# Kernel optimization log

Hardware: AMD Instinct MI355X
Metric: run time of the kernel (lower is better)

Reference implementation:

```python
import jax, jax.numpy as jnp
from jax import lax
import numpy as np

_DN = ('NCHW', 'OIHW', 'NCHW')


def _upfirdn2d(x, f, up, down, padding, gain, flip_filter):
    """Reference upfirdn2d with a separable 1-D FIR filter f. padding=(px0,px1,py0,py1)."""
    N, C, H, W = x.shape
    if up > 1:
        # zero-stuff upsample
        x = x.reshape(N, C, H, 1, W, 1)
        x = jnp.pad(x, ((0, 0), (0, 0), (0, 0), (0, up - 1), (0, 0), (0, up - 1)))
        x = x.reshape(N, C, H * up, W * up)
    px0, px1, py0, py1 = padding
    x = jnp.pad(x, ((0, 0), (0, 0), (max(py0, 0), max(py1, 0)), (max(px0, 0), max(px1, 0))))
    x = x[:, :, max(-py0, 0): x.shape[2] - max(-py1, 0), max(-px0, 0): x.shape[3] - max(-px1, 0)]
    # 1-D filter gets gain**(ndim/2) per pass -> total gain after H and W passes
    f = f * (gain ** (f.ndim / 2))
    if not flip_filter:
        f = f[::-1]
    f = f.astype(x.dtype)
    kt = f.shape[0]
    # separable depthwise FIR: vertical then horizontal
    fy = jnp.broadcast_to(f.reshape(1, 1, kt, 1), (C, 1, kt, 1))
    x = lax.conv_general_dilated(x, fy, (1, 1), 'VALID', feature_group_count=C, dimension_numbers=_DN)
    fx = jnp.broadcast_to(f.reshape(1, 1, 1, kt), (C, 1, 1, kt))
    x = lax.conv_general_dilated(x, fx, (1, 1), 'VALID', feature_group_count=C, dimension_numbers=_DN)
    if down > 1:
        x = x[:, :, ::down, ::down]
    return x


def conv2d_resample(x, w, f, up, down, padding, groups, flip_weight, flip_filter):
    out_c, in_cpg, kh, kw = w.shape
    fh = fw = f.shape[0]
    px0 = px1 = py0 = py1 = int(padding)
    # adjust padding for up/downsampling (StyleGAN2-ADA conv2d_resample)
    if up > 1:
        px0 += (fw + up - 1) // 2
        px1 += (fw - up) // 2
        py0 += (fh + up - 1) // 2
        py1 += (fh - up) // 2
    if down > 1:
        px0 += (fw - down + 1) // 2
        px1 += (fw - down) // 2
        py0 += (fh - down + 1) // 2
        py1 += (fh - down) // 2
    # generic path: upsample+FIR+pad, grouped conv, then FIR+downsample
    ff = f if up > 1 else jnp.ones((1,), x.dtype)
    x = _upfirdn2d(x, ff, up, 1, (px0, px1, py0, py1), up * up, flip_filter)
    if not flip_weight:
        w = w[:, :, ::-1, ::-1]
    y = lax.conv_general_dilated(x, w, (1, 1), 'VALID', feature_group_count=groups, dimension_numbers=_DN)
    if down > 1:
        y = _upfirdn2d(y, f, 1, down, (0, 0, 0, 0), 1, flip_filter)
    return y


def setup_inputs() -> dict:
    key = jax.random.key(0)
    k1, k2, k3 = jax.random.split(key, 3)
    x = jax.random.normal(k1, (4, 128, 256, 256), dtype=jnp.float32)
    f = jax.random.uniform(k2, (4,), dtype=jnp.float32)
    f = f / jnp.sum(f)  # normalized FIR taps (like binomial [1,3,3,1]/8)
    w = jax.random.normal(k3, (128, 16, 3, 3), dtype=jnp.float32) * 0.05
    return {"x": x, "f": f, "w": w, "up": 2, "down": 1, "padding": 1,
            "groups": 8, "flip_weight": 1, "flip_filter": 0}


def reference(x, f, w, up, down, padding, groups, flip_weight, flip_filter):
    return conv2d_resample(x, w, f, up, down, padding, groups, flip_weight, flip_filter)
```

## Files before the change

### kernel.cpp

```cpp
#include <hip/hip_runtime.h>

#define N_BATCH 4
#define OC 128
#define ICPG 16
#define GROUPS 8
#define H 256
#define W 256

__device__ float g_weff[OC * ICPG * 9 * 4];


__global__ void prep_weff(const float* __restrict__ w, const float* __restrict__ f) {
    int t = blockIdx.x * 256 + threadIdx.x;
    if (t >= OC * ICPG) return;
    float wl[9];
#pragma unroll
    for (int i = 0; i < 9; i++) wl[i] = w[t * 9 + i];
    float fl[4];
#pragma unroll
    for (int i = 0; i < 4; i++) fl[i] = f[i];
    float* out = g_weff + t * 36;
#pragma unroll
    for (int r = 0; r < 3; r++) {
#pragma unroll
        for (int s = 0; s < 3; s++) {
#pragma unroll
            for (int pi = 0; pi < 2; pi++) {
#pragma unroll
                for (int pj = 0; pj < 2; pj++) {
                    float acc = 0.f;
#pragma unroll
                    for (int dy = 0; dy < 3; dy++) {
                        int fy = pi + dy - 2 * (r - 1);
                        if (fy < 0 || fy > 3) continue;
#pragma unroll
                        for (int dx = 0; dx < 3; dx++) {
                            int fx = pj + dx - 2 * (s - 1);
                            if (fx < 0 || fx > 3) continue;
                            acc += wl[dy * 3 + dx] * fl[fy] * fl[fx];
                        }
                    }
                    out[(r * 3 + s) * 4 + pi * 2 + pj] = 4.f * acc;
                }
            }
        }
    }
}

__global__ __launch_bounds__(256) void conv_fused(const float* __restrict__ x,
                                                  float* __restrict__ y) {
    const int bj = threadIdx.x;
    const int bi = blockIdx.x;
    const int o  = blockIdx.y;
    const int n  = blockIdx.z;
    const int g  = o >> 4;

    const float* xb = x + ((size_t)(n * OC + g * ICPG)) * (H * W);
    const float* wp = g_weff + (size_t)o * ICPG * 36;

    float acc0 = 0.f, acc1 = 0.f, acc2 = 0.f, acc3 = 0.f;

    for (int c = 0; c < ICPG; c++) {
        const float* xc = xb + (size_t)c * (H * W);
#pragma unroll
        for (int r = 0; r < 3; r++) {
            const int iy = bi + r - 1;
            const bool vy = (unsigned)iy < (unsigned)H;
            const float* xr = xc + iy * W;
#pragma unroll
            for (int s = 0; s < 3; s++) {
                const int ix = bj + s - 1;
                const float xv = (vy && (unsigned)ix < (unsigned)W) ? xr[ix] : 0.f;
                const float4 wv = *(const float4*)(wp + ((c * 3 + r) * 3 + s) * 4);
                acc0 += xv * wv.x;
                acc1 += xv * wv.y;
                acc2 += xv * wv.z;
                acc3 += xv * wv.w;
            }
        }
    }

    float* yb = y + (((size_t)(n * OC + o) * 512) + 2 * bi) * 512 + 2 * bj;
    *(float2*)(yb)       = make_float2(acc0, acc1);
    *(float2*)(yb + 512) = make_float2(acc2, acc3);
}

extern "C" void kernel_launch(void* const* d_in, const int* in_sizes, int n_in,
                              void* d_out, int out_size, void* d_ws, size_t ws_size,
                              hipStream_t stream) {
    const float* x = (const float*)d_in[0];
    const float* f = (const float*)d_in[1];
    const float* w = (const float*)d_in[2];
    float* y = (float*)d_out;

    hipLaunchKernelGGL(prep_weff, dim3(8), dim3(256), 0, stream, w, f);

    dim3 grid(H, OC, N_BATCH);
    hipLaunchKernelGGL(conv_fused, grid, dim3(256), 0, stream, x, y);
}
```

Before: 1.222 ms.

## Register-block 4 columns per thread with float4 loads and wave shuffles for halos

Each thread now computes four adjacent input columns, so one float4 load per input row replaces nine scalar loads. The left and right halo values come from neighbouring lanes via shuffles. Each weight float4 is reused across four columns and results are written with float4 stores. Blocks become 4 waves, each looping over 4 rows, which cuts the grid by 16x. The aim is less global load traffic and fewer instructions, in exchange for more registers per thread and fewer blocks.

```diff
diff --git a/kernel.cpp b/kernel.cpp
--- a/kernel.cpp
+++ b/kernel.cpp
@@ -6,6 +6,8 @@
 #define GROUPS 8
 #define H 256
 #define W 256
+#define TR 16
+#define RPW 4
 
 __device__ float g_weff[OC * ICPG * 9 * 4];
 
@@ -49,40 +51,68 @@
 
 __global__ __launch_bounds__(256) void conv_fused(const float* __restrict__ x,
                                                   float* __restrict__ y) {
-    const int bj = threadIdx.x;
-    const int bi = blockIdx.x;
-    const int o  = blockIdx.y;
-    const int n  = blockIdx.z;
-    const int g  = o >> 4;
+    const int lane = threadIdx.x & 63;
+    const int wid  = threadIdx.x >> 6;
+    const int rowt = blockIdx.x;
+    const int o    = blockIdx.y;
+    const int n    = blockIdx.z;
+    const int g    = o >> 4;
 
+    const int bj4 = lane << 2;
     const float* xb = x + ((size_t)(n * OC + g * ICPG)) * (H * W);
     const float* wp = g_weff + (size_t)o * ICPG * 36;
 
-    float acc0 = 0.f, acc1 = 0.f, acc2 = 0.f, acc3 = 0.f;
+    const int bi0 = rowt * TR + wid * RPW;
 
-    for (int c = 0; c < ICPG; c++) {
-        const float* xc = xb + (size_t)c * (H * W);
+#pragma unroll 1
+    for (int rr = 0; rr < RPW; rr++) {
+        const int bi = bi0 + rr;
+
+        float acc[4][4];
 #pragma unroll
-        for (int r = 0; r < 3; r++) {
-            const int iy = bi + r - 1;
-            const bool vy = (unsigned)iy < (unsigned)H;
-            const float* xr = xc + iy * W;
+        for (int j = 0; j < 4; j++)
 #pragma unroll
-            for (int s = 0; s < 3; s++) {
-                const int ix = bj + s - 1;
-                const float xv = (vy && (unsigned)ix < (unsigned)W) ? xr[ix] : 0.f;
-                const float4 wv = *(const float4*)(wp + ((c * 3 + r) * 3 + s) * 4);
-                acc0 += xv * wv.x;
-                acc1 += xv * wv.y;
-                acc2 += xv * wv.z;
-                acc3 += xv * wv.w;
+            for (int ph = 0; ph < 4; ph++) acc[j][ph] = 0.f;
+
+#pragma unroll 2
+        for (int c = 0; c < ICPG; c++) {
+            const float* xc = xb + (size_t)c * (H * W);
+            const float* wc = wp + c * 36;
+#pragma unroll
+            for (int r = 0; r < 3; r++) {
+                const int iy = bi + r - 1;
+                float4 v;
+                if ((unsigned)iy < (unsigned)H) {
+                    v = *(const float4*)(xc + (size_t)iy * W + bj4);
+                } else {
+                    v = make_float4(0.f, 0.f, 0.f, 0.f);
+                }
+                float xl = __shfl_up(v.w, 1);
+                if (lane == 0) xl = 0.f;
+                float xr = __shfl_down(v.x, 1);
+                if (lane == 63) xr = 0.f;
+                const float xw[6] = {xl, v.x, v.y, v.z, v.w, xr};
+#pragma unroll
+                for (int s = 0; s < 3; s++) {
+                    const float4 wv = *(const float4*)(wc + (r * 3 + s) * 4);
+#pragma unroll
+                    for (int j = 0; j < 4; j++) {
+                        const float xv = xw[j + s];
+                        acc[j][0] += xv * wv.x;
+                        acc[j][1] += xv * wv.y;
+                        acc[j][2] += xv * wv.z;
+                        acc[j][3] += xv * wv.w;
+                    }
+                }
             }
         }
+
+        float* yb = y + (((size_t)(n * OC + o) * (2 * H)) + 2 * bi) * (2 * W) + 2 * bj4;
+        *(float4*)(yb)             = make_float4(acc[0][0], acc[0][1], acc[1][0], acc[1][1]);
+        *(float4*)(yb + 4)         = make_float4(acc[2][0], acc[2][1], acc[3][0], acc[3][1]);
+        *(float4*)(yb + 2 * W)     = make_float4(acc[0][2], acc[0][3], acc[1][2], acc[1][3]);
+        *(float4*)(yb + 2 * W + 4) = make_float4(acc[2][2], acc[2][3], acc[3][2], acc[3][3]);
     }
-
-    float* yb = y + (((size_t)(n * OC + o) * 512) + 2 * bi) * 512 + 2 * bj;
-    *(float2*)(yb)       = make_float2(acc0, acc1);
-    *(float2*)(yb + 512) = make_float2(acc2, acc3);
 }
 
 extern "C" void kernel_launch(void* const* d_in, const int* in_sizes, int n_in,
@@ -95,6 +125,6 @@
 
     hipLaunchKernelGGL(prep_weff, dim3(8), dim3(256), 0, stream, w, f);
 
-    dim3 grid(H, OC, N_BATCH);
+    dim3 grid(H / TR, OC, N_BATCH);
     hipLaunchKernelGGL(conv_fused, grid, dim3(256), 0, stream, x, y);
 }
```

After: 1.135 ms. -7.1%, faster.
